# Kernel optimization log

Measured on AMD Instinct MI355X. Metric: run time of the kernel, lower is better.

The kernel has to match this reference:

```python
import jax, jax.numpy as jnp
import numpy as np

H, W, C = 56, 56, 192
WS, SS = 7, 3          # window_size, shift_size
NH, HD = 6, 32         # num_heads, head_dim
N = WS * WS            # tokens per window = 49
HIDDEN = 4 * C
EPS = 1e-5


def _rel_pos_index():
    coords = np.stack(np.meshgrid(np.arange(WS), np.arange(WS), indexing='ij'))  # (2,ws,ws)
    flat = coords.reshape(2, -1)
    rel = flat[:, :, None] - flat[:, None, :]            # (2,N,N)
    rel = rel.transpose(1, 2, 0)
    rel[:, :, 0] += WS - 1
    rel[:, :, 1] += WS - 1
    rel[:, :, 0] *= 2 * WS - 1
    return rel.sum(-1)                                   # (N,N) int


def _attn_mask():
    img = np.zeros((H, W))
    cnt = 0
    for hs in (slice(0, -WS), slice(-WS, -SS), slice(-SS, None)):
        for ws_ in (slice(0, -WS), slice(-WS, -SS), slice(-SS, None)):
            img[hs, ws_] = cnt
            cnt += 1
    mw = img.reshape(H // WS, WS, W // WS, WS).transpose(0, 2, 1, 3).reshape(-1, N)  # (nW,N)
    diff = mw[:, None, :] - mw[:, :, None]
    return np.where(diff != 0, -100.0, 0.0).astype(np.float32)  # (nW,N,N)


REL_IDX = jnp.asarray(_rel_pos_index())
ATTN_MASK = jnp.asarray(_attn_mask())


def _ln(x, w, b):
    mu = x.mean(-1, keepdims=True)
    var = ((x - mu) ** 2).mean(-1, keepdims=True)
    return (x - mu) * jax.lax.rsqrt(var + EPS) * w + b


def _window_partition(x):
    # (B,H,W,C) -> (B*nW, N, C)
    B = x.shape[0]
    x = x.reshape(B, H // WS, WS, W // WS, WS, C)
    x = x.transpose(0, 1, 3, 2, 4, 5)
    return x.reshape(-1, N, C)


def _window_reverse(win, B):
    # (B*nW, N, C) -> (B,H,W,C)
    x = win.reshape(B, H // WS, W // WS, WS, WS, C)
    x = x.transpose(0, 1, 3, 2, 4, 5)
    return x.reshape(B, H, W, C)


def setup_inputs() -> dict:
    key = jax.random.key(0)
    ks = jax.random.split(key, 16)
    s = 0.02
    return {
        'x': jax.random.normal(ks[0], (64, H * W, C), jnp.float32),
        'norm1_w': jnp.ones((C,), jnp.float32),
        'norm1_b': jnp.zeros((C,), jnp.float32),
        'qkv_w': jax.random.normal(ks[1], (C, 3 * C), jnp.float32) * s,
        'qkv_b': jnp.zeros((3 * C,), jnp.float32),
        'rpb': jax.random.normal(ks[2], ((2 * WS - 1) ** 2, NH), jnp.float32) * s,
        'proj_w': jax.random.normal(ks[3], (C, C), jnp.float32) * s,
        'proj_b': jnp.zeros((C,), jnp.float32),
        'norm2_w': jnp.ones((C,), jnp.float32),
        'norm2_b': jnp.zeros((C,), jnp.float32),
        'fc1_w': jax.random.normal(ks[4], (C, HIDDEN), jnp.float32) * s,
        'fc1_b': jnp.zeros((HIDDEN,), jnp.float32),
        'fc2_w': jax.random.normal(ks[5], (HIDDEN, C), jnp.float32) * s,
        'fc2_b': jnp.zeros((C,), jnp.float32),
    }


def reference(x, norm1_w, norm1_b, qkv_w, qkv_b, rpb, proj_w, proj_b,
              norm2_w, norm2_b, fc1_w, fc1_b, fc2_w, fc2_b):
    B = x.shape[0]
    nW = (H // WS) * (W // WS)
    shortcut = x
    h = _ln(x, norm1_w, norm1_b).reshape(B, H, W, C)
    # cyclic shift
    h = jnp.roll(h, shift=(-SS, -SS), axis=(1, 2))
    xw = _window_partition(h)                                   # (B*nW, N, C)
    # windowed MHA
    qkv = (xw @ qkv_w + qkv_b).reshape(-1, N, 3, NH, HD).transpose(2, 0, 3, 1, 4)
    q, k, v = qkv[0], qkv[1], qkv[2]                            # (Bn, NH, N, HD)
    scale = HD ** -0.5
    attn = jnp.einsum('bhnd,bhmd->bhnm', q * scale, k)          # (Bn, NH, N, N)
    bias = rpb[REL_IDX.reshape(-1)].reshape(N, N, NH).transpose(2, 0, 1)
    attn = attn + bias[None]
    attn = attn.reshape(B, nW, NH, N, N) + ATTN_MASK[None, :, None]
    attn = jax.nn.softmax(attn.reshape(-1, NH, N, N), axis=-1)
    out = jnp.einsum('bhnm,bhmd->bhnd', attn, v)
    out = out.transpose(0, 2, 1, 3).reshape(-1, N, C)
    out = out @ proj_w + proj_b
    # reverse windows + un-shift
    h = _window_reverse(out, B)
    h = jnp.roll(h, shift=(SS, SS), axis=(1, 2)).reshape(B, H * W, C)
    x = shortcut + h
    # MLP (exact GELU, as torch nn.GELU default)
    m = _ln(x, norm2_w, norm2_b)
    m = jax.nn.gelu(m @ fc1_w + fc1_b, approximate=False)
    m = m @ fc2_w + fc2_b
    return x + m
```

## Files before the change

### kernel.cpp

```cpp
#include <hip/hip_runtime.h>
#include <hip/hip_bf16.h>

typedef __hip_bfloat16 bf16;
typedef __attribute__((ext_vector_type(8))) short short8;
typedef __attribute__((ext_vector_type(4))) float floatx4;

__device__ __forceinline__ floatx4 mfma16(short8 a, short8 b, floatx4 c) {
  return __builtin_amdgcn_mfma_f32_16x16x32_bf16(a, b, c, 0, 0, 0);
}

__device__ __forceinline__ float wave_sum(float v) {
#pragma unroll
  for (int off = 1; off < 64; off <<= 1) v += __shfl_xor(v, off);
  return v;
}

__device__ __forceinline__ void gload16(const void* g, void* l) {
  __builtin_amdgcn_global_load_lds(
      (const __attribute__((address_space(1))) unsigned int*)g,
      (__attribute__((address_space(3))) unsigned int*)l, 16, 0, 0);
}

__device__ __forceinline__ short8 lds_frag(const char* base, int row, int kb) {
  return *(const short8*)(base + row * 384 + (kb ^ ((row & 7) << 4)));
}

__global__ __launch_bounds__(256) void k_wt(const float* __restrict__ w,
                                            bf16* __restrict__ wt, int K, int N) {
  int id = blockIdx.x * 256 + threadIdx.x;
  if (id < K * N) {
    int n = id / K;
    int k = id - n * K;
    wt[id] = __float2bfloat16(w[(long)k * N + n]);
  }
}

template <bool GATHER>
__global__ __launch_bounds__(256) void k_ln(const float* __restrict__ xin,
                                            const float* __restrict__ w,
                                            const float* __restrict__ b,
                                            bf16* __restrict__ out) {
  const int lane = threadIdx.x & 63;
  const long row = (long)blockIdx.x * 4 + (threadIdx.x >> 6);
  long srow;
  if (GATHER) {
    int win = (int)(row / 49);
    int token = (int)(row - (long)win * 49);
    int bimg = win >> 6, wi = (win & 63) >> 3, wj = win & 7;
    int ti = token / 7, tj = token - ti * 7;
    int h = wi * 7 + ti + 3; if (h >= 56) h -= 56;
    int ww = wj * 7 + tj + 3; if (ww >= 56) ww -= 56;
    srow = (long)bimg * 3136 + h * 56 + ww;
  } else {
    srow = row;
  }
  const float* src = xin + srow * 192;
  float v0 = src[lane], v1 = src[lane + 64], v2 = src[lane + 128];
  float mu = wave_sum(v0 + v1 + v2) * (1.f / 192.f);
  float d0 = v0 - mu, d1 = v1 - mu, d2 = v2 - mu;
  float var = wave_sum(d0 * d0 + d1 * d1 + d2 * d2) * (1.f / 192.f);
  float rs = rsqrtf(var + 1e-5f);
  bf16* dst = out + row * 192;
  dst[lane]       = __float2bfloat16(d0 * rs * w[lane] + b[lane]);
  dst[lane + 64]  = __float2bfloat16(d1 * rs * w[lane + 64] + b[lane + 64]);
  dst[lane + 128] = __float2bfloat16(d2 * rs * w[lane + 128] + b[lane + 128]);
}

template <int EPI>
__global__ __launch_bounds__(256, 3) void k_gemm(const bf16* __restrict__ A,
                                                 const bf16* __restrict__ Bt,
                                                 const float* __restrict__ bias,
                                                 bf16* __restrict__ Cbf,
                                                 float* __restrict__ Cfp,
                                                 const float* __restrict__ res,
                                                 int Ncols, int K, long row0) {
  __shared__ __align__(16) char As[64 * 384];
  __shared__ __align__(16) char Bs[64 * 384];
  const int t = threadIdx.x;
  const int lane = t & 63, wid = t >> 6;
  const int lanelo = lane & 15, quad = lane >> 4;
  const long m0 = (long)blockIdx.x * 64;
  const int n0 = blockIdx.y * 64;
  const int wm = (wid >> 1) * 32, wn = (wid & 1) * 32;

  floatx4 acc[2][2];
#pragma unroll
  for (int i = 0; i < 2; i++)
#pragma unroll
    for (int j = 0; j < 2; j++) acc[i][j] = (floatx4){0.f, 0.f, 0.f, 0.f};

  const char* Ab = (const char*)(A + m0 * (long)K);
  const char* Bb = (const char*)(Bt + (long)n0 * K);
  const int ldab = 2 * K;

  for (int k0b = 0; k0b < 2 * K; k0b += 384) {
    __syncthreads();
#pragma unroll
    for (int i = 0; i < 6; i++) {
      int c = i * 256 + t;
      int r = c / 24;
      int j = c - r * 24;
      int be = (j * 16) ^ ((r & 7) << 4);
      gload16(Ab + (long)r * ldab + k0b + be, As + c * 16);
      gload16(Bb + (long)r * ldab + k0b + be, Bs + c * 16);
    }
    __syncthreads();

#pragma unroll
    for (int kk = 0; kk < 6; kk++) {
      const int kb = kk * 64 + quad * 16;
      short8 a0 = lds_frag(As, wm + lanelo, kb);
      short8 a1 = lds_frag(As, wm + 16 + lanelo, kb);
      short8 b0 = lds_frag(Bs, wn + lanelo, kb);
      short8 b1 = lds_frag(Bs, wn + 16 + lanelo, kb);
      acc[0][0] = mfma16(a0, b0, acc[0][0]);
      acc[0][1] = mfma16(a0, b1, acc[0][1]);
      acc[1][0] = mfma16(a1, b0, acc[1][0]);
      acc[1][1] = mfma16(a1, b1, acc[1][1]);
    }
  }

#pragma unroll
  for (int mi = 0; mi < 2; mi++) {
#pragma unroll
    for (int reg = 0; reg < 4; reg++) {
      const long r = m0 + wm + mi * 16 + quad * 4 + reg;
      long orow = r;
      if (EPI == 2) {
        const long rg = row0 + r;
        int win = (int)(rg / 49);
        int token = (int)(rg - (long)win * 49);
        int bimg = win >> 6, wi = (win & 63) >> 3, wj = win & 7;
        int ti = token / 7, tj = token - ti * 7;
        int h = wi * 7 + ti + 3; if (h >= 56) h -= 56;
        int ww = wj * 7 + tj + 3; if (ww >= 56) ww -= 56;
        orow = (long)bimg * 3136 + h * 56 + ww;
      }
#pragma unroll
      for (int ni = 0; ni < 2; ni++) {
        const int c = n0 + wn + ni * 16 + lanelo;
        float v = acc[mi][ni][reg] + bias[c];
        if (EPI == 0) {
          Cbf[r * Ncols + c] = __float2bfloat16(v);
        } else if (EPI == 1) {
          v = 0.5f * v * (1.f + erff(v * 0.70710678118654752f));
          Cbf[r * Ncols + c] = __float2bfloat16(v);
        } else if (EPI == 2) {
          Cfp[orow * 192 + c] = v + res[orow * 192 + c];
        } else {
          Cfp[r * 192 + c] = v + res[r * 192 + c];
        }
      }
    }
  }
}

__global__ __launch_bounds__(256, 2) void k_attn(const bf16* __restrict__ qkv,
                                                 const float* __restrict__ rpb,
                                                 bf16* __restrict__ out) {
  __shared__ __align__(16) bf16 smem[4 * 7424];
  const int t = threadIdx.x, lane = t & 63, wid = t >> 6;
  const int lanelo = lane & 15, quad = lane >> 4;
  const int unit = blockIdx.x * 4 + wid;
  const int win = unit / 6, head = unit - win * 6;
  bf16* Qs = smem + wid * 7424;
  bf16* Ks = Qs + 2560;
  bf16* Vt = Qs + 5120;
  bf16* Ps = Qs;
  const long rowbase = (long)win * 49;
  const bf16* base = qkv + rowbase * 576 + head * 32;

  for (int idx = lane; idx < 196; idx += 64) {
    int tok = idx >> 2, ch = (idx & 3) * 8;
    *(uint4*)(&Qs[tok * 40 + ch]) = *(const uint4*)(base + (long)tok * 576 + ch);
    *(uint4*)(&Ks[tok * 40 + ch]) = *(const uint4*)(base + (long)tok * 576 + 192 + ch);
    union { uint4 u; bf16 h[8]; } tv;
    tv.u = *(const uint4*)(base + (long)tok * 576 + 384 + ch);
#pragma unroll
    for (int jj = 0; jj < 8; jj++) Vt[(ch + jj) * 72 + tok] = tv.h[jj];
  }
  for (int idx = lane; idx < 480; idx += 64) {
    int d = idx / 15, c = 49 + (idx - d * 15);
    Vt[d * 72 + c] = __float2bfloat16(0.f);
  }
  __syncthreads();

  floatx4 aS[4][4];
#pragma unroll
  for (int mi = 0; mi < 4; mi++)
#pragma unroll
    for (int ni = 0; ni < 4; ni++) aS[mi][ni] = (floatx4){0.f, 0.f, 0.f, 0.f};
  {
    short8 aq[4], bk[4];
#pragma unroll
    for (int mi = 0; mi < 4; mi++)
      aq[mi] = *(const short8*)(&Qs[(mi * 16 + lanelo) * 40 + quad * 8]);
#pragma unroll
    for (int ni = 0; ni < 4; ni++)
      bk[ni] = *(const short8*)(&Ks[(ni * 16 + lanelo) * 40 + quad * 8]);
#pragma unroll
    for (int mi = 0; mi < 4; mi++)
#pragma unroll
      for (int ni = 0; ni < 4; ni++) aS[mi][ni] = mfma16(aq[mi], bk[ni], aS[mi][ni]);
  }

  const int w_in = win & 63, wiw = w_in >> 3, wjw = w_in & 7;
  int cTi[4], cTj[4], cLab[4];
  bool cval[4];
#pragma unroll
  for (int ni = 0; ni < 4; ni++) {
    int j = ni * 16 + lanelo;
    cval[ni] = (j < 49);
    if (j > 48) j = 48;
    int ti = j / 7, tj = j - ti * 7;
    int rr = wiw * 7 + ti, cc = wjw * 7 + tj;
    cTi[ni] = ti;
    cTj[ni] = tj;
    cLab[ni] = ((rr < 49) ? 0 : (rr < 53 ? 1 : 2)) * 3 +
               ((cc < 49) ? 0 : (cc < 53 ? 1 : 2));
  }

  const float scale = 0.17677669529663687f;
  float rinv[16];
#pragma unroll
  for (int mi = 0; mi < 4; mi++) {
#pragma unroll
    for (int reg = 0; reg < 4; reg++) {
      int i = mi * 16 + quad * 4 + reg;
      if (i > 48) i = 48;
      int ti = i / 7, tj = i - ti * 7;
      int rr = wiw * 7 + ti, cc = wjw * 7 + tj;
      int rlab = ((rr < 49) ? 0 : (rr < 53 ? 1 : 2)) * 3 +
                 ((cc < 49) ? 0 : (cc < 53 ? 1 : 2));
      float sv[4];
      float mx = -1e30f;
#pragma unroll
      for (int ni = 0; ni < 4; ni++) {
        float s;
        if (cval[ni]) {
          int ridx = (ti - cTi[ni] + 6) * 13 + (tj - cTj[ni] + 6);
          float bb = rpb[ridx * 6 + head];
          if (rlab != cLab[ni]) bb -= 100.f;
          s = aS[mi][ni][reg] * scale + bb;
        } else {
          s = -1e30f;
        }
        sv[ni] = s;
        mx = fmaxf(mx, s);
      }
      mx = fmaxf(mx, __shfl_xor(mx, 1));
      mx = fmaxf(mx, __shfl_xor(mx, 2));
      mx = fmaxf(mx, __shfl_xor(mx, 4));
      mx = fmaxf(mx, __shfl_xor(mx, 8));
      float sum = 0.f;
#pragma unroll
      for (int ni = 0; ni < 4; ni++) {
        float p = __expf(sv[ni] - mx);
        sv[ni] = p;
        sum += p;
      }
      sum += __shfl_xor(sum, 1);
      sum += __shfl_xor(sum, 2);
      sum += __shfl_xor(sum, 4);
      sum += __shfl_xor(sum, 8);
      rinv[mi * 4 + reg] = 1.f / sum;
#pragma unroll
      for (int ni = 0; ni < 4; ni++) aS[mi][ni][reg] = sv[ni];
    }
  }
  __syncthreads();

#pragma unroll
  for (int mi = 0; mi < 4; mi++)
#pragma unroll
    for (int ni = 0; ni < 4; ni++)
#pragma unroll
      for (int reg = 0; reg < 4; reg++) {
        int i = mi * 16 + quad * 4 + reg, j = ni * 16 + lanelo;
        Ps[i * 72 + j] = __float2bfloat16(aS[mi][ni][reg]);
      }
  __syncthreads();

  floatx4 aO[4][2];
#pragma unroll
  for (int mi = 0; mi < 4; mi++)
#pragma unroll
    for (int ni = 0; ni < 2; ni++) aO[mi][ni] = (floatx4){0.f, 0.f, 0.f, 0.f};
#pragma unroll
  for (int k0 = 0; k0 < 64; k0 += 32) {
    short8 ap[4], bv[2];
#pragma unroll
    for (int mi = 0; mi < 4; mi++)
      ap[mi] = *(const short8*)(&Ps[(mi * 16 + lanelo) * 72 + k0 + quad * 8]);
#pragma unroll
    for (int ni = 0; ni < 2; ni++)
      bv[ni] = *(const short8*)(&Vt[(ni * 16 + lanelo) * 72 + k0 + quad * 8]);
#pragma unroll
    for (int mi = 0; mi < 4; mi++)
#pragma unroll
      for (int ni = 0; ni < 2; ni++) aO[mi][ni] = mfma16(ap[mi], bv[ni], aO[mi][ni]);
  }

#pragma unroll
  for (int mi = 0; mi < 4; mi++)
#pragma unroll
    for (int reg = 0; reg < 4; reg++) {
      int i = mi * 16 + quad * 4 + reg;
      if (i < 49) {
        float rv = rinv[mi * 4 + reg];
#pragma unroll
        for (int ni = 0; ni < 2; ni++) {
          int d = ni * 16 + lanelo;
          out[(rowbase + i) * 192 + head * 32 + d] =
              __float2bfloat16(aO[mi][ni][reg] * rv);
        }
      }
    }
}

extern "C" void kernel_launch(void* const* d_in, const int* in_sizes, int n_in,
                              void* d_out, int out_size, void* d_ws, size_t ws_size,
                              hipStream_t stream) {
  const float* x     = (const float*)d_in[0];
  const float* n1w   = (const float*)d_in[1];
  const float* n1b   = (const float*)d_in[2];
  const float* qkvw  = (const float*)d_in[3];
  const float* qkvb  = (const float*)d_in[4];
  const float* rpb   = (const float*)d_in[5];
  const float* projw = (const float*)d_in[6];
  const float* projb = (const float*)d_in[7];
  const float* n2w   = (const float*)d_in[8];
  const float* n2b   = (const float*)d_in[9];
  const float* fc1w  = (const float*)d_in[10];
  const float* fc1b  = (const float*)d_in[11];
  const float* fc2w  = (const float*)d_in[12];
  const float* fc2b  = (const float*)d_in[13];
  float* outf = (float*)d_out;

  const long CR = 50176;
  const int  NCH = 4;

  char* ws = (char*)d_ws;
  bf16* xw      = (bf16*)(ws + 0);
  bf16* qkvC    = (bf16*)(ws + 77070336LL);
  bf16* attC    = (bf16*)(ws + 134873088LL);
  bf16* hidC    = (bf16*)(ws + 77070336LL);
  bf16* m       = xw;
  bf16* wt_qkv  = (bf16*)(ws + 154140672LL);
  bf16* wt_proj = (bf16*)(ws + 154140672LL + 221184LL);
  bf16* wt_fc1  = (bf16*)(ws + 154140672LL + 294912LL);
  bf16* wt_fc2  = (bf16*)(ws + 154140672LL + 589824LL);

  k_wt<<<dim3((192 * 576 + 255) / 256), 256, 0, stream>>>(qkvw, wt_qkv, 192, 576);
  k_wt<<<dim3((192 * 192 + 255) / 256), 256, 0, stream>>>(projw, wt_proj, 192, 192);
  k_wt<<<dim3((192 * 768 + 255) / 256), 256, 0, stream>>>(fc1w, wt_fc1, 192, 768);
  k_wt<<<dim3((768 * 192 + 255) / 256), 256, 0, stream>>>(fc2w, wt_fc2, 768, 192);

  k_ln<true><<<dim3(50176), 256, 0, stream>>>(x, n1w, n1b, xw);

  for (int c = 0; c < NCH; c++) {
    const long r0 = c * CR;
    k_gemm<0><<<dim3(784, 9), 256, 0, stream>>>(xw + r0 * 192, wt_qkv, qkvb,
                                                qkvC, nullptr, nullptr, 576, 192, 0);
    k_attn<<<dim3(1536), 256, 0, stream>>>(qkvC, rpb, attC);
    k_gemm<2><<<dim3(784, 3), 256, 0, stream>>>(attC, wt_proj, projb, nullptr,
                                                outf, x, 192, 192, r0);
  }

  k_ln<false><<<dim3(50176), 256, 0, stream>>>(outf, n2w, n2b, m);

  for (int c = 0; c < NCH; c++) {
    const long r0 = c * CR;
    k_gemm<1><<<dim3(784, 12), 256, 0, stream>>>(m + r0 * 192, wt_fc1, fc1b,
                                                 hidC, nullptr, nullptr, 768, 192, 0);
    k_gemm<3><<<dim3(784, 3), 256, 0, stream>>>(hidC, wt_fc2, fc2b, nullptr,
                                                outf + r0 * 192, outf + r0 * 192,
                                                192, 768, 0);
  }
}
```

Baseline: 1.097 ms.

## Fuse LayerNorm2, FC1+GELU and FC2+residual into one MLP kernel

Replaces the separate LayerNorm kernel and the chunked FC1/FC2 GEMM launches with one kernel per 64-row tile. The kernel normalizes rows into LDS, streams FC1 weight slices and the matching FC2 weight slices, applies GELU into a small LDS hidden tile, and accumulates FC2 in registers before adding the residual in place. This removes the global round trips of the normalized activations and the 768-wide hidden tensor and cuts launches. In exchange, every block re-reads all MLP weights, uses about 96KB of LDS, and each stage is synchronized with no overlap between weight loads and compute.

```diff
diff --git a/kernel.cpp b/kernel.cpp
--- a/kernel.cpp
+++ b/kernel.cpp
@@ -23,6 +23,9 @@
 
 __device__ __forceinline__ short8 lds_frag(const char* base, int row, int kb) {
   return *(const short8*)(base + row * 384 + (kb ^ ((row & 7) << 4)));
+}
+__device__ __forceinline__ short8 lds_frag128(const char* base, int row, int kb) {
+  return *(const short8*)(base + row * 128 + (kb ^ ((row & 7) << 4)));
 }
 
 __global__ __launch_bounds__(256) void k_wt(const float* __restrict__ w,
@@ -155,6 +158,126 @@
   }
 }
 
+__global__ __launch_bounds__(256, 2) void k_mlp(float* xres,
+                                                const float* __restrict__ lw,
+                                                const float* __restrict__ lb,
+                                                const bf16* __restrict__ w1t,
+                                                const float* __restrict__ b1,
+                                                const bf16* __restrict__ w2t,
+                                                const float* __restrict__ b2) {
+  __shared__ __align__(16) char As[64 * 384];
+  __shared__ __align__(16) char B1s[64 * 384];
+  __shared__ __align__(16) char B2s[192 * 128];
+  __shared__ __align__(16) char Hs[64 * 128];
+  const int t = threadIdx.x, lane = t & 63, wid = t >> 6;
+  const int lanelo = lane & 15, quad = lane >> 4;
+  const long row0 = (long)blockIdx.x * 64;
+  const int wm = (wid >> 1) * 32;
+  const int wn = (wid & 1) * 32;
+  const int wn2 = (wid & 1) * 96;
+
+  for (int i = 0; i < 16; i++) {
+    int r = wid * 16 + i;
+    const float* src = xres + (row0 + r) * 192;
+    float v0 = src[lane], v1 = src[lane + 64], v2 = src[lane + 128];
+    float mu = wave_sum(v0 + v1 + v2) * (1.f / 192.f);
+    float d0 = v0 - mu, d1 = v1 - mu, d2 = v2 - mu;
+    float var = wave_sum(d0 * d0 + d1 * d1 + d2 * d2) * (1.f / 192.f);
+    float rs = rsqrtf(var + 1e-5f);
+    int sw = (r & 7) << 4;
+    *(bf16*)(As + r * 384 + ((2 * lane) ^ sw)) =
+        __float2bfloat16(d0 * rs * lw[lane] + lb[lane]);
+    *(bf16*)(As + r * 384 + ((128 + 2 * lane) ^ sw)) =
+        __float2bfloat16(d1 * rs * lw[lane + 64] + lb[lane + 64]);
+    *(bf16*)(As + r * 384 + ((256 + 2 * lane) ^ sw)) =
+        __float2bfloat16(d2 * rs * lw[lane + 128] + lb[lane + 128]);
+  }
+
+  floatx4 acc2[2][6];
+#pragma unroll
+  for (int mi = 0; mi < 2; mi++)
+#pragma unroll
+    for (int ni = 0; ni < 6; ni++) acc2[mi][ni] = (floatx4){0.f, 0.f, 0.f, 0.f};
+
+  for (int nc = 0; nc < 12; nc++) {
+#pragma unroll
+    for (int i = 0; i < 6; i++) {
+      int c = i * 256 + t;
+      int r1 = c / 24, j1 = c - r1 * 24;
+      gload16((const char*)w1t + (long)(nc * 64 + r1) * 384 +
+                  ((j1 * 16) ^ ((r1 & 7) << 4)),
+              B1s + c * 16);
+      int r2 = c >> 3, j2 = c & 7;
+      gload16((const char*)w2t + (long)r2 * 1536 + nc * 128 +
+                  ((j2 * 16) ^ ((r2 & 7) << 4)),
+              B2s + c * 16);
+    }
+    __syncthreads();
+
+    floatx4 acc1[2][2];
+#pragma unroll
+    for (int mi = 0; mi < 2; mi++)
+#pragma unroll
+      for (int ni = 0; ni < 2; ni++) acc1[mi][ni] = (floatx4){0.f, 0.f, 0.f, 0.f};
+#pragma unroll
+    for (int kk = 0; kk < 6; kk++) {
+      const int kb = kk * 64 + quad * 16;
+      short8 a0 = lds_frag(As, wm + lanelo, kb);
+      short8 a1 = lds_frag(As, wm + 16 + lanelo, kb);
+      short8 b0 = lds_frag(B1s, wn + lanelo, kb);
+      short8 b1f = lds_frag(B1s, wn + 16 + lanelo, kb);
+      acc1[0][0] = mfma16(a0, b0, acc1[0][0]);
+      acc1[0][1] = mfma16(a0, b1f, acc1[0][1]);
+      acc1[1][0] = mfma16(a1, b0, acc1[1][0]);
+      acc1[1][1] = mfma16(a1, b1f, acc1[1][1]);
+    }
+
+#pragma unroll
+    for (int ni = 0; ni < 2; ni++) {
+      const int cl = wn + ni * 16 + lanelo;
+      const float b1v = b1[nc * 64 + cl];
+#pragma unroll
+      for (int mi = 0; mi < 2; mi++)
+#pragma unroll
+        for (int reg = 0; reg < 4; reg++) {
+          int r = wm + mi * 16 + quad * 4 + reg;
+          float v = acc1[mi][ni][reg] + b1v;
+          v = 0.5f * v * (1.f + erff(v * 0.70710678118654752f));
+          *(bf16*)(Hs + r * 128 + ((2 * cl) ^ ((r & 7) << 4))) =
+              __float2bfloat16(v);
+        }
+    }
+    __syncthreads();
+
+#pragma unroll
+    for (int ks = 0; ks < 2; ks++) {
+      const int kb = ks * 64 + quad * 16;
+      short8 ha0 = lds_frag128(Hs, wm + lanelo, kb);
+      short8 ha1 = lds_frag128(Hs, wm + 16 + lanelo, kb);
+#pragma unroll
+      for (int ni = 0; ni < 6; ni++) {
+        short8 bv = lds_frag128(B2s, wn2 + ni * 16 + lanelo, kb);
+        acc2[0][ni] = mfma16(ha0, bv, acc2[0][ni]);
+        acc2[1][ni] = mfma16(ha1, bv, acc2[1][ni]);
+      }
+    }
+    __syncthreads();
+  }
+
+#pragma unroll
+  for (int mi = 0; mi < 2; mi++)
+#pragma unroll
+    for (int ni = 0; ni < 6; ni++) {
+      const int c = wn2 + ni * 16 + lanelo;
+      const float b2v = b2[c];
+#pragma unroll
+      for (int reg = 0; reg < 4; reg++) {
+        const long g = (row0 + wm + mi * 16 + quad * 4 + reg) * 192 + c;
+        xres[g] = acc2[mi][ni][reg] + b2v + xres[g];
+      }
+    }
+}
+
 __global__ __launch_bounds__(256, 2) void k_attn(const bf16* __restrict__ qkv,
                                                  const float* __restrict__ rpb,
                                                  bf16* __restrict__ out) {
@@ -344,8 +467,6 @@
   bf16* xw      = (bf16*)(ws + 0);
   bf16* qkvC    = (bf16*)(ws + 77070336LL);
   bf16* attC    = (bf16*)(ws + 134873088LL);
-  bf16* hidC    = (bf16*)(ws + 77070336LL);
-  bf16* m       = xw;
   bf16* wt_qkv  = (bf16*)(ws + 154140672LL);
   bf16* wt_proj = (bf16*)(ws + 154140672LL + 221184LL);
   bf16* wt_fc1  = (bf16*)(ws + 154140672LL + 294912LL);
@@ -367,14 +488,6 @@
                                                 outf, x, 192, 192, r0);
   }
 
-  k_ln<false><<<dim3(50176), 256, 0, stream>>>(outf, n2w, n2b, m);
-
-  for (int c = 0; c < NCH; c++) {
-    const long r0 = c * CR;
-    k_gemm<1><<<dim3(784, 12), 256, 0, stream>>>(m + r0 * 192, wt_fc1, fc1b,
-                                                 hidC, nullptr, nullptr, 768, 192, 0);
-    k_gemm<3><<<dim3(784, 3), 256, 0, stream>>>(hidC, wt_fc2, fc2b, nullptr,
-                                                outf + r0 * 192, outf + r0 * 192,
-                                                192, 768, 0);
-  }
-}
+  k_mlp<<<dim3(3136), 256, 0, stream>>>(outf, n2w, n2b, wt_fc1, fc1b,
+                                        wt_fc2, fc2b);
+}
```

Result: faster. 1.015 ms (-7.5%).
